# Optimization experiments

Measured on AMD Instinct MI355X. Metric: run time of the kernel, lower is better.

Reference implementation:

```python
import jax, jax.numpy as jnp
import numpy as np


def setup_inputs() -> dict:
    key = jax.random.key(0)
    ks = jax.random.split(key, 5)
    B, S, D = 2, 2048, 1024
    std = 0.02
    return {
        "x": jax.random.normal(ks[0], (B, S, D), dtype=jnp.float32),
        "Wq": jax.random.normal(ks[1], (D, D), dtype=jnp.float32) * std,
        "Wk": jax.random.normal(ks[2], (D, D), dtype=jnp.float32) * std,
        "Wv": jax.random.normal(ks[3], (D, D), dtype=jnp.float32) * std,
        "Wo": jax.random.normal(ks[4], (D, D), dtype=jnp.float32) * std,
        "num_heads": 16,
        "window_size": 512,
    }


def reference(x, Wq, Wk, Wv, Wo, num_heads, window_size):
    B, S, D = x.shape
    H = num_heads
    d = D // H
    scale = d ** (-0.5)

    # QKV projections (torch Linear: y = x @ W.T), split heads -> b h s d
    def proj(W):
        return (x @ W.T).reshape(B, S, H, d).transpose(0, 2, 1, 3)

    q, k, v = proj(Wq), proj(Wk), proj(Wv)

    # [B, H, S, S] scores (faithful to the dense SDPA fallback)
    scores = jnp.einsum("bhsd,bhtd->bhst", q, k) * scale

    # sliding-window causal mask: col <= row and row - col < window_size
    pos = jnp.arange(S)
    row, col = pos[:, None], pos[None, :]
    mask = (col <= row) & (row - col < window_size)  # [S, S]
    scores = jnp.where(mask[None, None], scores, -jnp.inf)

    attn = jax.nn.softmax(scores, axis=-1)
    out = jnp.einsum("bhst,bhtd->bhsd", attn, v)  # b h s d
    out = out.transpose(0, 2, 1, 3).reshape(B, S, D)  # merge heads
    return out @ Wo.T
```

## Files before the change

kernel.cpp:

```cpp
#include <hip/hip_runtime.h>
#include <cstdint>

typedef uint16_t u16;
typedef __attribute__((ext_vector_type(8))) short short8;
typedef __attribute__((ext_vector_type(4))) float f32x4;

__device__ __forceinline__ u16 f2bf(float f) {
  uint32_t u = __float_as_uint(f);
  u += 0x7fff + ((u >> 16) & 1);
  return (u16)(u >> 16);
}
__device__ __forceinline__ uint32_t pk2bf(float a, float b) {
  uint32_t ua = __float_as_uint(a) + 0x8000u;
  uint32_t ub = __float_as_uint(b) + 0x8000u;
  return (ua >> 16) | (ub & 0xFFFF0000u);
}

#define GLL16(gp, lp) __builtin_amdgcn_global_load_lds( \
    (__attribute__((address_space(1))) void*)(gp), \
    (__attribute__((address_space(3))) void*)(lp), 16, 0, 0)

#define SBAR()       __builtin_amdgcn_s_barrier()
#define WAIT_LGKM0() asm volatile("s_waitcnt lgkmcnt(0)" ::: "memory")
#define WAIT_VM(N)   asm volatile("s_waitcnt vmcnt(" #N ")" ::: "memory")
#define MEMBAR()     asm volatile("" ::: "memory")

__global__ void cvt_all(const float* __restrict__ x,  const float* __restrict__ wq,
                        const float* __restrict__ wk, const float* __restrict__ wv,
                        const float* __restrict__ wo,
                        u16* __restrict__ xb, u16* __restrict__ wcat, u16* __restrict__ wob) {
  int i = blockIdx.x * 256 + threadIdx.x;
  const float4* src; ushort4* dst; int off; float sc = 1.0f;
  if (i < 1048576)      { src = (const float4*)x;  dst = (ushort4*)xb;              off = i; }
  else if (i < 1310720) { src = (const float4*)wq; dst = (ushort4*)wcat;            off = i - 1048576;
                          sc = 0.18033688011112042f; }
  else if (i < 1572864) { src = (const float4*)wk; dst = (ushort4*)wcat + 262144;   off = i - 1310720; }
  else if (i < 1835008) { src = (const float4*)wv; dst = (ushort4*)wcat + 524288;   off = i - 1572864; }
  else                  { src = (const float4*)wo; dst = (ushort4*)wob;             off = i - 1835008; }
  float4 v = src[off];
  ushort4 o;
  o.x = f2bf(v.x * sc); o.y = f2bf(v.y * sc); o.z = f2bf(v.z * sc); o.w = f2bf(v.w * sc);
  dst[off] = o;
}

template<int BM, int OUT_BF16, int OCC>
__global__ __launch_bounds__(256, OCC) void gemm_t(const u16* __restrict__ A,
                                                   const u16* __restrict__ B,
                                                   void* __restrict__ Cout,
                                                   int N, int K, int ntN) {
  constexpr int MF = BM / 32;
  __shared__ u16 smA[2][BM * 64];
  __shared__ u16 smB[2][128 * 64];
  const int tid  = threadIdx.x;
  const int lane = tid & 63, w = tid >> 6;
  const int wr = w >> 1, wc = w & 1;
  const int g = lane >> 4, lr = lane & 15;

  const int cpx = gridDim.x >> 3;
  const int id  = blockIdx.x;
  const int sw  = (id & 7) * cpx + (id >> 3);
  const int row0 = (sw / ntN) * BM, col0 = (sw % ntN) * 128;
  const int T = K >> 6;

  f32x4 acc[MF][4];
  #pragma unroll
  for (int i = 0; i < MF; ++i)
    #pragma unroll
    for (int j = 0; j < 4; ++j) acc[i][j] = (f32x4){0.f, 0.f, 0.f, 0.f};

  auto STAGE = [&](int kt, int bufi) {
    #pragma unroll
    for (int j = 0; j < BM / 32; ++j) {
      int r  = j * 32 + w * 8 + (lane >> 3);
      int sb = ((lane & 7) << 4) ^ ((r & 7) << 4);
      GLL16(A + (size_t)(row0 + r) * K + kt * 64 + (sb >> 1),
            &smA[bufi][(size_t)(j * 32 + w * 8) * 64]);
    }
    #pragma unroll
    for (int j = 0; j < 4; ++j) {
      int r  = j * 32 + w * 8 + (lane >> 3);
      int sb = ((lane & 7) << 4) ^ ((r & 7) << 4);
      GLL16(B + (size_t)(col0 + r) * K + kt * 64 + (sb >> 1),
            &smB[bufi][(size_t)(j * 32 + w * 8) * 64]);
    }
  };
  auto WVM_STEADY = [&]() {
    if constexpr (BM == 128) { WAIT_VM(8); } else { WAIT_VM(6); }
  };

  STAGE(0, 0); STAGE(1, 1);
  WVM_STEADY(); SBAR(); MEMBAR();

  for (int t = 0; t < T; ++t) {
    const int cur = t & 1;
    short8 a[MF][2], b[4][2];
    #pragma unroll
    for (int mm = 0; mm < MF; ++mm)
      #pragma unroll
      for (int kh = 0; kh < 2; ++kh) {
        int row = wr * (BM / 2) + mm * 16 + lr;
        int col = (kh * 64 + g * 16) ^ ((row & 7) << 4);
        a[mm][kh] = *(const short8*)((const char*)&smA[cur][0] + row * 128 + col);
      }
    #pragma unroll
    for (int nn = 0; nn < 4; ++nn)
      #pragma unroll
      for (int kh = 0; kh < 2; ++kh) {
        int row = wc * 64 + nn * 16 + lr;
        int col = (kh * 64 + g * 16) ^ ((row & 7) << 4);
        b[nn][kh] = *(const short8*)((const char*)&smB[cur][0] + row * 128 + col);
      }
    WAIT_LGKM0(); MEMBAR(); SBAR(); MEMBAR();

    if (t + 2 < T) STAGE(t + 2, cur);

    __builtin_amdgcn_s_setprio(1);
    #pragma unroll
    for (int kh = 0; kh < 2; ++kh)
      #pragma unroll
      for (int mm = 0; mm < MF; ++mm)
        #pragma unroll
        for (int nn = 0; nn < 4; ++nn)
          acc[mm][nn] = __builtin_amdgcn_mfma_f32_16x16x32_bf16(
              a[mm][kh], b[nn][kh], acc[mm][nn], 0, 0, 0);
    __builtin_amdgcn_s_setprio(0);

    if (t + 1 < T) {
      if (t + 2 < T) { WVM_STEADY(); } else { WAIT_VM(0); }
      SBAR(); MEMBAR();
    }
  }

  #pragma unroll
  for (int i = 0; i < MF; ++i)
    #pragma unroll
    for (int j = 0; j < 4; ++j)
      #pragma unroll
      for (int ri = 0; ri < 4; ++ri) {
        int rr = row0 + wr * (BM / 2) + i * 16 + g * 4 + ri;
        int cc = col0 + wc * 64 + j * 16 + lr;
        if (OUT_BF16) ((u16*)Cout)[(size_t)rr * N + cc] = f2bf(acc[i][j][ri]);
        else          ((float*)Cout)[(size_t)rr * N + cc] = acc[i][j][ri];
      }
}

__global__ __launch_bounds__(256, 3) void attn_swa(const u16* __restrict__ QKV, u16* __restrict__ O) {
  const int S = 2048;
  const int qb = blockIdx.x * 128;
  const int b = blockIdx.y >> 4, h = blockIdx.y & 15;
  const int tid = threadIdx.x;
  const int lane = tid & 63, w = tid >> 6;
  const int g = lane >> 4, lr = lane & 15;

  __shared__ u16 Klds[2][64 * 64];
  __shared__ u16 Vt[2][64][72];
  __shared__ u16 Plds[4][32][72];

  const u16* Qb = QKV + (size_t)b * S * 3072 + h * 64;
  const u16* Kb = QKV + (size_t)b * S * 3072 + 1024 + h * 64;
  const u16* Vb = QKV + (size_t)b * S * 3072 + 2048 + h * 64;

  const int qw = qb + w * 32;
  short8 qf[2][2];
  #pragma unroll
  for (int qg = 0; qg < 2; ++qg)
    #pragma unroll
    for (int kh = 0; kh < 2; ++kh)
      qf[qg][kh] = *(const short8*)(Qb + (size_t)(qw + qg * 16 + lr) * 3072 + kh * 32 + g * 8);

  float ls[2] = {0.f, 0.f};
  f32x4 accO[2][4];
  #pragma unroll
  for (int qg = 0; qg < 2; ++qg)
    #pragma unroll
    for (int i = 0; i < 4; ++i) accO[qg][i] = (f32x4){0.f, 0.f, 0.f, 0.f};

  int ks = qb - 511; if (ks < 0) ks = 0; ks &= ~63;
  const int ke = qb + 127;
  const int nt = ((ke - ks) >> 6) + 1;

  short8 vreg0, vreg1;

  auto STAGE_K = [&](int kb, int buf) {
    #pragma unroll
    for (int c = 0; c < 2; ++c) {
      int r  = c * 32 + w * 8 + (lane >> 3);
      int sb = ((lane & 7) << 4) ^ ((r & 7) << 4);
      const u16* gp = Kb + (size_t)(kb + r) * 3072 + (sb >> 1);
      u16* lp = Klds[buf] + c * 2048 + w * 512;
      GLL16(gp, lp);
    }
  };
  auto LOAD_V = [&](int kb) {
    vreg0 = *(const short8*)(Vb + (size_t)(kb + lane) * 3072 + w * 8);
    vreg1 = *(const short8*)(Vb + (size_t)(kb + lane) * 3072 + w * 8 + 32);
  };
  auto WRITE_V = [&](int buf) {
    #pragma unroll
    for (int j = 0; j < 8; ++j) Vt[buf][w * 8 + j][lane]      = (u16)vreg0[j];
    #pragma unroll
    for (int j = 0; j < 8; ++j) Vt[buf][w * 8 + 32 + j][lane] = (u16)vreg1[j];
  };

  LOAD_V(ks); MEMBAR();
  STAGE_K(ks, 0); MEMBAR();
  WAIT_VM(0); MEMBAR();
  SBAR(); MEMBAR();
  WRITE_V(0);

  int cur = 0, kb = ks;
  for (int t = 0; t < nt; ++t, kb += 64) {
    const int nxt = cur ^ 1;
    const bool more = (t + 1 < nt);
    if (more) { LOAD_V(kb + 64); MEMBAR(); STAGE_K(kb + 64, nxt); MEMBAR(); }

    const bool active = (kb <= qw + 31) && (kb + 63 >= qw - 511);
    if (active) {
      float p[2][4][4];
      #pragma unroll
      for (int st = 0; st < 4; ++st) {
        f32x4 c4[2];
        c4[0] = (f32x4){0.f, 0.f, 0.f, 0.f};
        c4[1] = (f32x4){0.f, 0.f, 0.f, 0.f};
        int r = st * 16 + lr;
        int swz = (r & 7) << 4;
        const char* krow = (const char*)(Klds[cur]) + r * 128;
        short8 kf0 = *(const short8*)(krow + ((g * 16) ^ swz));
        short8 kf1 = *(const short8*)(krow + ((64 + g * 16) ^ swz));
        __builtin_amdgcn_s_setprio(1);
        c4[0] = __builtin_amdgcn_mfma_f32_16x16x32_bf16(kf0, qf[0][0], c4[0], 0, 0, 0);
        c4[1] = __builtin_amdgcn_mfma_f32_16x16x32_bf16(kf0, qf[1][0], c4[1], 0, 0, 0);
        c4[0] = __builtin_amdgcn_mfma_f32_16x16x32_bf16(kf1, qf[0][1], c4[0], 0, 0, 0);
        c4[1] = __builtin_amdgcn_mfma_f32_16x16x32_bf16(kf1, qf[1][1], c4[1], 0, 0, 0);
        __builtin_amdgcn_s_setprio(0);
        #pragma unroll
        for (int ri = 0; ri < 4; ++ri) { p[0][st][ri] = c4[0][ri]; p[1][st][ri] = c4[1][ri]; }
      }

      #pragma unroll
      for (int qg = 0; qg < 2; ++qg) {
        const int q0 = qw + qg * 16;
        const bool clean = (kb + 63 <= q0) && (q0 + 15 - kb < 512);
        if (clean) {
          #pragma unroll
          for (int st = 0; st < 4; ++st)
            #pragma unroll
            for (int ri = 0; ri < 4; ++ri)
              p[qg][st][ri] = __builtin_amdgcn_exp2f(p[qg][st][ri]);
        } else {
          const int base = q0 + lr - kb;
          #pragma unroll
          for (int st = 0; st < 4; ++st)
            #pragma unroll
            for (int ri = 0; ri < 4; ++ri) {
              float e = __builtin_amdgcn_exp2f(p[qg][st][ri]);
              p[qg][st][ri] = ((uint32_t)(base - (st * 16 + g * 4 + ri)) < 512u) ? e : 0.f;
            }
        }
        float s = 0.f;
        #pragma unroll
        for (int st = 0; st < 4; ++st)
          #pragma unroll
          for (int ri = 0; ri < 4; ++ri) s += p[qg][st][ri];
        s += __shfl_xor(s, 16);
        s += __shfl_xor(s, 32);
        ls[qg] += s;

        #pragma unroll
        for (int st = 0; st < 4; ++st) {
          uint2 u2;
          u2.x = pk2bf(p[qg][st][0], p[qg][st][1]);
          u2.y = pk2bf(p[qg][st][2], p[qg][st][3]);
          *(uint2*)(&Plds[w][qg * 16 + lr][st * 16 + g * 4]) = u2;
        }
      }
    }

    if (more) { WAIT_VM(0); MEMBAR(); }
    WAIT_LGKM0(); MEMBAR();
    SBAR(); MEMBAR();
    if (more) WRITE_V(nxt);

    if (active) {
      short8 pf[2][2];
      #pragma unroll
      for (int qg = 0; qg < 2; ++qg) {
        pf[qg][0] = *(const short8*)(&Plds[w][qg * 16 + lr][g * 8]);
        pf[qg][1] = *(const short8*)(&Plds[w][qg * 16 + lr][32 + g * 8]);
      }
      __builtin_amdgcn_s_setprio(1);
      #pragma unroll
      for (int dt = 0; dt < 4; ++dt) {
        short8 vf0 = *(const short8*)(&Vt[cur][dt * 16 + lr][g * 8]);
        short8 vf1 = *(const short8*)(&Vt[cur][dt * 16 + lr][32 + g * 8]);
        accO[0][dt] = __builtin_amdgcn_mfma_f32_16x16x32_bf16(pf[0][0], vf0, accO[0][dt], 0, 0, 0);
        accO[1][dt] = __builtin_amdgcn_mfma_f32_16x16x32_bf16(pf[1][0], vf0, accO[1][dt], 0, 0, 0);
        accO[0][dt] = __builtin_amdgcn_mfma_f32_16x16x32_bf16(pf[0][1], vf1, accO[0][dt], 0, 0, 0);
        accO[1][dt] = __builtin_amdgcn_mfma_f32_16x16x32_bf16(pf[1][1], vf1, accO[1][dt], 0, 0, 0);
      }
      __builtin_amdgcn_s_setprio(0);
    }
    cur = nxt;
  }

  #pragma unroll
  for (int qg = 0; qg < 2; ++qg) {
    float lsq[4];
    #pragma unroll
    for (int ri = 0; ri < 4; ++ri) lsq[ri] = __shfl(ls[qg], g * 4 + ri);
    #pragma unroll
    for (int dt = 0; dt < 4; ++dt)
      #pragma unroll
      for (int ri = 0; ri < 4; ++ri) {
        int qi = qw + qg * 16 + g * 4 + ri;
        O[(size_t)(b * S + qi) * 1024 + h * 64 + dt * 16 + lr] = f2bf(accO[qg][dt][ri] / lsq[ri]);
      }
  }
}

extern "C" void kernel_launch(void* const* d_in, const int* in_sizes, int n_in,
                              void* d_out, int out_size, void* d_ws, size_t ws_size,
                              hipStream_t stream) {
  const float* x  = (const float*)d_in[0];
  const float* Wq = (const float*)d_in[1];
  const float* Wk = (const float*)d_in[2];
  const float* Wv = (const float*)d_in[3];
  const float* Wo = (const float*)d_in[4];

  char* ws = (char*)d_ws;
  u16* xb   = (u16*)(ws);
  u16* Wcat = (u16*)(ws + (8  << 20));
  u16* Wob  = (u16*)(ws + (14 << 20));
  u16* QKV  = (u16*)(ws + (16 << 20));
  u16* Oatt = (u16*)(ws + (40 << 20));

  cvt_all<<<8192, 256, 0, stream>>>(x, Wq, Wk, Wv, Wo, xb, Wcat, Wob);
  gemm_t<64, 1, 3><<<1536, 256, 0, stream>>>(xb, Wcat, QKV, 3072, 1024, 24);
  attn_swa<<<dim3(16, 32), 256, 0, stream>>>(QKV, Oatt);
  gemm_t<64, 0, 3><<<512, 256, 0, stream>>>(Oatt, Wob, d_out, 1024, 1024, 8);
}
```

Baseline: 92.10 us.

## Replace QKV projection GEMM with 256x256-tile 8-wave pipelined kernel

Adds a dedicated 256x256 tile GEMM with 512 threads, double-buffered LDS staging via global_load_lds, an interleaved load/MFMA schedule with barriers and setprio, and uses it for the QKV projection (192 blocks instead of 1536 small-tile blocks). The larger tile raises data reuse per LDS load and reduces global traffic. The risk is that 192 blocks leave some of the 256 CUs idle, and the output stores are scalar and strided. The output GEMM's occupancy hint also changes from 3 to 2.

```diff
diff --git a/kernel.cpp b/kernel.cpp
--- a/kernel.cpp
+++ b/kernel.cpp
@@ -41,6 +41,128 @@
   ushort4 o;
   o.x = f2bf(v.x * sc); o.y = f2bf(v.y * sc); o.z = f2bf(v.z * sc); o.w = f2bf(v.w * sc);
   dst[off] = o;
+}
+
+__global__ __launch_bounds__(512, 1) void gemm256(const u16* __restrict__ A,
+                                                  const u16* __restrict__ B,
+                                                  u16* __restrict__ Cp) {
+  __shared__ u16 sm[2][2][256 * 64];
+  const int tid  = threadIdx.x;
+  const int lane = tid & 63, w = tid >> 6;
+  const int wr = w >> 2, wc = w & 3;
+  const int g = lane >> 4, lr = lane & 15;
+
+  const int id = blockIdx.x;
+  const int sw = (id & 7) * 24 + (id >> 3);
+  const int row0 = (sw % 16) * 256;
+  const int col0 = (sw / 16) * 256;
+
+  f32x4 acc[8][4];
+  #pragma unroll
+  for (int m = 0; m < 8; ++m)
+    #pragma unroll
+    for (int n = 0; n < 4; ++n) acc[m][n] = (f32x4){0.f, 0.f, 0.f, 0.f};
+
+  auto STAGE = [&](int kt, int ab, int half) {
+    if (kt >= 16) return;
+    const u16* __restrict__ src = ab ? B : A;
+    const int rb = (ab ? col0 : row0) + half * 128;
+    u16* lds = &sm[kt & 1][ab][half * 128 * 64];
+    #pragma unroll
+    for (int j = 0; j < 2; ++j) {
+      int r  = j * 64 + w * 8 + (lane >> 3);
+      int sb = ((lane & 7) << 4) ^ ((r & 7) << 4);
+      GLL16(src + (size_t)(rb + r) * 1024 + kt * 64 + (sb >> 1),
+            lds + (size_t)(j * 512 + w * 64) * 8);
+    }
+  };
+
+  short8 a[8][2], b[4][2];
+  auto RDA = [&](int buf, int m0) {
+    #pragma unroll
+    for (int mm = 0; mm < 4; ++mm)
+      #pragma unroll
+      for (int kh = 0; kh < 2; ++kh) {
+        int row = wr * 128 + (m0 + mm) * 16 + lr;
+        int col = (kh * 64 + g * 16) ^ ((row & 7) << 4);
+        a[m0 + mm][kh] = *(const short8*)((const char*)&sm[buf][0][0] + row * 128 + col);
+      }
+  };
+  auto RDB = [&](int buf, int n0) {
+    #pragma unroll
+    for (int nn = 0; nn < 2; ++nn)
+      #pragma unroll
+      for (int kh = 0; kh < 2; ++kh) {
+        int row = wc * 64 + (n0 + nn) * 16 + lr;
+        int col = (kh * 64 + g * 16) ^ ((row & 7) << 4);
+        b[n0 + nn][kh] = *(const short8*)((const char*)&sm[buf][1][0] + row * 128 + col);
+      }
+  };
+  auto QUAD = [&](int m0, int n0) {
+    __builtin_amdgcn_s_setprio(1);
+    #pragma unroll
+    for (int kh = 0; kh < 2; ++kh)
+      #pragma unroll
+      for (int mm = 0; mm < 4; ++mm)
+        #pragma unroll
+        for (int nn = 0; nn < 2; ++nn)
+          acc[m0 + mm][n0 + nn] = __builtin_amdgcn_mfma_f32_16x16x32_bf16(
+              a[m0 + mm][kh], b[n0 + nn][kh], acc[m0 + mm][n0 + nn], 0, 0, 0);
+    __builtin_amdgcn_s_setprio(0);
+  };
+
+  STAGE(0, 0, 0); STAGE(0, 0, 1); STAGE(0, 1, 0); STAGE(0, 1, 1);
+  STAGE(1, 0, 0); STAGE(1, 0, 1);
+  WAIT_VM(4); SBAR(); MEMBAR();
+
+  for (int i = 0; i < 8; ++i) {
+    const int T = 2 * i;
+    RDA(0, 0); RDB(0, 0); STAGE(T + 1, 1, 0); MEMBAR();
+    SBAR(); WAIT_LGKM0(); MEMBAR();
+    QUAD(0, 0);
+    MEMBAR(); SBAR(); MEMBAR();
+    RDA(0, 4); STAGE(T + 1, 1, 1); MEMBAR();
+    SBAR(); WAIT_LGKM0(); MEMBAR();
+    QUAD(4, 0);
+    MEMBAR(); SBAR(); MEMBAR();
+    RDB(0, 2); STAGE(T + 2, 0, 0); MEMBAR();
+    SBAR(); WAIT_LGKM0(); MEMBAR();
+    QUAD(0, 2);
+    MEMBAR(); SBAR(); MEMBAR();
+    STAGE(T + 2, 0, 1); MEMBAR();
+    SBAR(); MEMBAR();
+    QUAD(4, 2);
+    if (i == 7) { WAIT_VM(0); } else { WAIT_VM(4); }
+    MEMBAR(); SBAR(); MEMBAR();
+    RDA(1, 0); RDB(1, 0); STAGE(T + 2, 1, 0); MEMBAR();
+    SBAR(); WAIT_LGKM0(); MEMBAR();
+    QUAD(0, 0);
+    MEMBAR(); SBAR(); MEMBAR();
+    RDA(1, 4); STAGE(T + 2, 1, 1); MEMBAR();
+    SBAR(); WAIT_LGKM0(); MEMBAR();
+    QUAD(4, 0);
+    MEMBAR(); SBAR(); MEMBAR();
+    RDB(1, 2); STAGE(T + 3, 0, 0); MEMBAR();
+    SBAR(); WAIT_LGKM0(); MEMBAR();
+    QUAD(0, 2);
+    MEMBAR(); SBAR(); MEMBAR();
+    STAGE(T + 3, 0, 1); MEMBAR();
+    SBAR(); MEMBAR();
+    QUAD(4, 2);
+    if (i == 7) { WAIT_VM(0); } else { WAIT_VM(4); }
+    MEMBAR(); SBAR(); MEMBAR();
+  }
+
+  #pragma unroll
+  for (int m = 0; m < 8; ++m)
+    #pragma unroll
+    for (int n = 0; n < 4; ++n)
+      #pragma unroll
+      for (int ri = 0; ri < 4; ++ri) {
+        int rr = row0 + wr * 128 + m * 16 + g * 4 + ri;
+        int cc = col0 + wc * 64 + n * 16 + lr;
+        Cp[(size_t)rr * 3072 + cc] = f2bf(acc[m][n][ri]);
+      }
 }
 
 template<int BM, int OUT_BF16, int OCC>
@@ -335,7 +457,7 @@
   u16* Oatt = (u16*)(ws + (40 << 20));
 
   cvt_all<<<8192, 256, 0, stream>>>(x, Wq, Wk, Wv, Wo, xb, Wcat, Wob);
-  gemm_t<64, 1, 3><<<1536, 256, 0, stream>>>(xb, Wcat, QKV, 3072, 1024, 24);
+  gemm256<<<192, 512, 0, stream>>>(xb, Wcat, QKV);
   attn_swa<<<dim3(16, 32), 256, 0, stream>>>(QKV, Oatt);
-  gemm_t<64, 0, 3><<<512, 256, 0, stream>>>(Oatt, Wob, d_out, 1024, 1024, 8);
-}
+  gemm_t<64, 0, 2><<<512, 256, 0, stream>>>(Oatt, Wob, d_out, 1024, 1024, 8);
+}
```

Measured after the change: 105.4 us. 1.14x slower.
